# Kernel optimization log

Hardware: AMD Instinct MI355X
Metric: run time of the kernel (lower is better)

## Reference

```python
import jax, jax.numpy as jnp
import numpy as np

N = 100000   # nodes
E = 400000   # edges
L = 128      # latent_size
LN_EPS = 1e-5


def _mlp(x, W1, b1, W2, b2, g=None, beta=None):
    # build_mlp_d: Linear -> ReLU -> Linear, optional trailing LayerNorm
    h = jax.nn.relu(x @ W1 + b1)
    y = h @ W2 + b2
    if g is not None:
        mu = y.mean(-1, keepdims=True)
        var = y.var(-1, keepdims=True)
        y = (y - mu) / jnp.sqrt(var + LN_EPS) * g + beta
    return y


def setup_inputs():
    key = jax.random.key(0)
    ks = iter(jax.random.split(key, 100))

    def nrm(shape, scale=1.0):
        return jax.random.normal(next(ks), shape, jnp.float32) * scale

    inp = {}
    inp["edge_index"] = jax.random.randint(next(ks), (2, E), 0, N, dtype=jnp.int32)
    for nm in ["senders_pos", "receivers_pos", "edge_dx", "edge_dt",
               "vector_a", "vector_b", "vector_c",
               "senders_v_t", "senders_v_tm1", "senders_w_t",
               "receivers_v_t", "receivers_v_tm1", "receivers_w_t"]:
        inp[nm] = nrm((E, 3))
    inp["edge_attr"] = nrm((E, 1))
    inp["node_latent"] = nrm((N, L))

    def mlp_p(pref, din, dh, dout, ln):
        inp[pref + "_W1"] = nrm((din, dh), 1.0 / np.sqrt(din))
        inp[pref + "_b1"] = jnp.zeros((dh,), jnp.float32)
        inp[pref + "_W2"] = nrm((dh, dout), 1.0 / np.sqrt(dh))
        inp[pref + "_b2"] = jnp.zeros((dout,), jnp.float32)
        if ln:
            inp[pref + "_g"] = jnp.ones((dout,), jnp.float32)
            inp[pref + "_b"] = jnp.zeros((dout,), jnp.float32)

    mlp_p("ef", 9, L, L, True)       # edge_feat_encoder
    mlp_p("ee", 3, L, L, True)       # edge_encoder
    mlp_p("ie", 3 * L, L, L, True)   # interaction_encoder
    mlp_p("i1", L, L, 3, False)      # i1_decoder
    mlp_p("i2", L, L, 3, False)      # i2_decoder
    mlp_p("fs", L, L, 1, False)      # f_scaler
    mlp_p("nw", L, L, 1, False)      # node_weight_decoder
    mlp_p("mi", L, L, 1, False)      # m_inv_decoder
    mlp_p("ii", L, L, 1, False)      # i_inv_decoder
    mlp_p("de", L, L, 1, False)      # dv_ext_decoder
    # bias node weights to ~1 so the r0ij denominator stays away from 0
    inp["nw_b2"] = jnp.ones((1,), jnp.float32)
    return inp


def reference(edge_index, senders_pos, receivers_pos, edge_dx, edge_dt, edge_attr,
              vector_a, vector_b, vector_c,
              senders_v_t, senders_v_tm1, senders_w_t,
              receivers_v_t, receivers_v_tm1, receivers_w_t, node_latent,
              ef_W1, ef_b1, ef_W2, ef_b2, ef_g, ef_b,
              ee_W1, ee_b1, ee_W2, ee_b2, ee_g, ee_b,
              ie_W1, ie_b1, ie_W2, ie_b2, ie_g, ie_b,
              i1_W1, i1_b1, i1_W2, i1_b2,
              i2_W1, i2_b1, i2_W2, i2_b2,
              fs_W1, fs_b1, fs_W2, fs_b2,
              nw_W1, nw_b1, nw_W2, nw_b2,
              mi_W1, mi_b1, mi_W2, mi_b2,
              ii_W1, ii_b1, ii_W2, ii_b2,
              de_W1, de_b1, de_W2, de_b2):
    senders, receivers = edge_index[0], edge_index[1]

    def dots(v):  # [E,3] dotted against the three edge-frame basis vectors -> [E,3]
        return jnp.stack([jnp.einsum('ej,ej->e', v, vector_a),
                          jnp.einsum('ej,ej->e', v, vector_b),
                          jnp.einsum('ej,ej->e', v, vector_c)], axis=1)

    # --- InteractionEncoder ---
    senders_features = jnp.concatenate(
        [dots(senders_v_t), dots(senders_v_tm1), dots(senders_w_t)], axis=1)   # [E,9]
    receivers_features = -jnp.concatenate(
        [dots(receivers_v_t), dots(receivers_v_tm1), dots(receivers_w_t)], axis=1)  # [E,9]

    edge_in = jnp.concatenate(
        [jnp.linalg.norm(edge_dx, axis=1, keepdims=True),
         jnp.linalg.norm(edge_dt, axis=1, keepdims=True),
         edge_attr], axis=1)                                                    # [E,3]
    edge_latent = _mlp(edge_in, ee_W1, ee_b1, ee_W2, ee_b2, ee_g, ee_b)
    senders_latent = _mlp(senders_features, ef_W1, ef_b1, ef_W2, ef_b2, ef_g, ef_b)
    receivers_latent = _mlp(receivers_features, ef_W1, ef_b1, ef_W2, ef_b2, ef_g, ef_b)

    interaction_in = jnp.concatenate(
        [senders_latent + receivers_latent,
         node_latent[senders] + node_latent[receivers],
         edge_latent], axis=1)                                                  # [E,3L]
    interaction_latent = _mlp(interaction_in, ie_W1, ie_b1, ie_W2, ie_b2, ie_g, ie_b)

    # --- InteractionDecoder ---
    coeff_f = _mlp(interaction_latent, i1_W1, i1_b1, i1_W2, i1_b2)  # [E,3]
    coeff_a = _mlp(interaction_latent, i2_W1, i2_b1, i2_W2, i2_b2)  # [E,3]
    node_weights = _mlp(node_latent, nw_W1, nw_b1, nw_W2, nw_b2)    # [N,1]
    lambda_ij = _mlp(interaction_latent, fs_W1, fs_b1, fs_W2, fs_b2)  # [E,1]

    fij = coeff_f[:, 0:1] * vector_a + coeff_f[:, 1:2] * vector_b + coeff_f[:, 2:3] * vector_c
    aij = coeff_a[:, 0:1] * vector_a + coeff_a[:, 1:2] * vector_b + coeff_a[:, 2:3] * vector_c
    ws = node_weights[senders]
    wr = node_weights[receivers]
    r0ij = (ws * senders_pos + wr * receivers_pos) / (ws + wr)
    tauij = aij - jnp.cross(receivers_pos - r0ij, fij) * lambda_ij

    # --- Node_Internal_Dv_Decoder ---
    m_inv = _mlp(node_latent, mi_W1, mi_b1, mi_W2, mi_b2)  # [N,1]
    i_inv = _mlp(node_latent, ii_W1, ii_b1, ii_W2, ii_b2)  # [N,1]
    out_fij = jax.ops.segment_sum(fij, receivers, num_segments=N)   # scatter_add
    node_dv_int = m_inv * out_fij + _mlp(node_latent, de_W1, de_b1, de_W2, de_b2)
    out_tij = jax.ops.segment_sum(tauij, receivers, num_segments=N)
    node_dw_int = i_inv * out_tij

    return (node_dv_int, node_dw_int, interaction_latent)
```

## Files before the change

kernel.cpp:

```cpp
#include <hip/hip_runtime.h>
#include <hip/hip_fp16.h>
#include <stdint.h>

#define E_EDGES 400000
#define N_NODES 100000

#define OW1P  ((size_t)0)
#define OW2P  ((size_t)98304)
#define OW1D  ((size_t)131072)
#define OW2D  ((size_t)229376)
#define OW1E  ((size_t)241664)
#define OW2E  ((size_t)249856)
#define OW1C  ((size_t)282624)
#define OW2C  ((size_t)290816)
#define OSLR  ((size_t)524288)
#define ONW   (OSLR + (size_t)E_EDGES * 64 * 4)
#define OMI   (ONW + (size_t)N_NODES * 4)
#define OII   (OMI + (size_t)N_NODES * 4)
#define ODE   (OII + (size_t)N_NODES * 4)
#define OFS   (ODE + (size_t)N_NODES * 4)
#define OTS   (OFS + (size_t)N_NODES * 12)
#define WSEND (OTS + (size_t)N_NODES * 12)

typedef __attribute__((ext_vector_type(8))) _Float16 f16x8;
typedef __attribute__((ext_vector_type(4))) float f32x4;

__device__ __forceinline__ uint32_t f2h(float f) {
  return (uint32_t)__half_as_ushort(__float2half(f));
}
__device__ __forceinline__ float wave_sum64(float v) {
#pragma unroll
  for (int off = 32; off > 0; off >>= 1) v += __shfl_xor(v, off, 64);
  return v;
}

__device__ __forceinline__ void gemv8(const float* __restrict__ W,
                                      const float* __restrict__ xb, int xstride,
                                      int Ka, int lane, float* a0, float* a1) {
#pragma unroll 2
  for (int i = 0; i < Ka; i += 4) {
    float w0[4], w1[4];
#pragma unroll
    for (int u = 0; u < 4; ++u) {
      w0[u] = W[(size_t)(i + u) * 128 + lane];
      w1[u] = W[(size_t)(i + u) * 128 + 64 + lane];
    }
#pragma unroll
    for (int r = 0; r < 8; ++r) {
#pragma unroll
      for (int u = 0; u < 4; ++u) {
        float xv = xb[r * xstride + i + u];
        a0[r] = fmaf(xv, w0[u], a0[r]);
        a1[r] = fmaf(xv, w1[u], a1[r]);
      }
    }
  }
}

__device__ __forceinline__ void copy8x128(const float* __restrict__ src,
                                          float* __restrict__ dst, int lane) {
#pragma unroll
  for (int t = 0; t < 4; ++t) {
    float4 v = ((const float4*)src)[lane + 64 * t];
    ((float4*)dst)[lane + 64 * t] = v;
  }
}

__global__ __launch_bounds__(256) void k_node(
    const float* __restrict__ NL,
    const float* __restrict__ nw_W1, const float* __restrict__ nw_b1,
    const float* __restrict__ nw_W2, const float* __restrict__ nw_b2,
    const float* __restrict__ mi_W1, const float* __restrict__ mi_b1,
    const float* __restrict__ mi_W2, const float* __restrict__ mi_b2,
    const float* __restrict__ ii_W1, const float* __restrict__ ii_b1,
    const float* __restrict__ ii_W2, const float* __restrict__ ii_b2,
    const float* __restrict__ de_W1, const float* __restrict__ de_b1,
    const float* __restrict__ de_W2, const float* __restrict__ de_b2,
    float* __restrict__ o_nw, float* __restrict__ o_mi, float* __restrict__ o_ii,
    float* __restrict__ o_de) {
  __shared__ float xb[4][8 * 128];
  int w = threadIdx.x >> 6, l = threadIdx.x & 63;
  int nb = blockIdx.x * 32 + w * 8;
  copy8x128(NL + (size_t)nb * 128, xb[w], l);
  __syncthreads();
  const float* W1s[4] = {nw_W1, mi_W1, ii_W1, de_W1};
  const float* B1[4] = {nw_b1, mi_b1, ii_b1, de_b1};
  const float* W2[4] = {nw_W2, mi_W2, ii_W2, de_W2};
  const float* B2[4] = {nw_b2, mi_b2, ii_b2, de_b2};
  float* OUT[4] = {o_nw, o_mi, o_ii, o_de};
#pragma unroll
  for (int m = 0; m < 4; ++m) {
    float b10 = B1[m][l], b11 = B1[m][l + 64];
    float a0[8], a1[8];
#pragma unroll
    for (int r = 0; r < 8; ++r) { a0[r] = b10; a1[r] = b11; }
    gemv8(W1s[m], xb[w], 128, 128, l, a0, a1);
    float w2a = W2[m][l], w2b = W2[m][l + 64];
    float b2 = B2[m][0];
    float y[8];
#pragma unroll
    for (int r = 0; r < 8; ++r) {
      float p = fmaxf(a0[r], 0.f) * w2a + fmaxf(a1[r], 0.f) * w2b;
      y[r] = wave_sum64(p) + b2;
    }
    if (l == 0) {
#pragma unroll
      for (int r = 0; r < 8; ++r) OUT[m][nb + r] = y[r];
    }
  }
}

__global__ __launch_bounds__(256) void k_prep(
    const float* __restrict__ W1, const float* __restrict__ W2,
    const float* __restrict__ i1W1, const float* __restrict__ i2W1,
    const float* __restrict__ fsW1,
    const float* __restrict__ i1W2, const float* __restrict__ i2W2,
    const float* __restrict__ fsW2,
    const float* __restrict__ efW1, const float* __restrict__ efW2,
    const float* __restrict__ eeW1, const float* __restrict__ eeW2,
    unsigned short* __restrict__ W1P, unsigned short* __restrict__ W2P,
    unsigned short* __restrict__ W1D, unsigned short* __restrict__ W2D,
    unsigned short* __restrict__ W1E, unsigned short* __restrict__ W2E,
    unsigned short* __restrict__ W1C, unsigned short* __restrict__ W2C) {
  int i = blockIdx.x * 256 + threadIdx.x;
  if (i < 12 * 128 * 32) {
    int kin = i & 31, c = (i >> 5) & 127, ks = i >> 12;
    int kx = ks * 32 + kin;
    int ko = (kx < 128) ? ((kx & 1) * 64 + (kx >> 1)) : kx;
    W1P[i] = (unsigned short)f2h(W1[(size_t)ko * 128 + c]);
  }
  if (i < 4 * 128 * 32) {
    int kin = i & 31, c = (i >> 5) & 127, ks = i >> 12;
    W2P[i] = (unsigned short)f2h(W2[(size_t)(ks * 32 + kin) * 128 + c]);
  }
  if (i < 4 * 384 * 32) {
    int kin = i & 31;
    int rest = i >> 5;
    int c = rest % 384;
    int ks = rest / 384;
    int k = ks * 32 + kin;
    int head = c >> 7, ch = c & 127;
    const float* Wh = head == 0 ? i1W1 : head == 1 ? i2W1 : fsW1;
    W1D[i] = (unsigned short)f2h(Wh[(size_t)k * 128 + ch]);
  }
  if (i < 12 * 16 * 32) {
    int kin = i & 31;
    int rest = i >> 5;
    int col = rest & 15;
    int ks = rest >> 4;
    int k = ks * 32 + kin;
    float v = 0.f;
    if (k < 128) { if (col < 3) v = i1W2[(size_t)k * 3 + col]; }
    else if (k < 256) { if (col >= 3 && col < 6) v = i2W2[(size_t)(k - 128) * 3 + (col - 3)]; }
    else { if (col == 6) v = fsW2[k - 256]; }
    W2D[i] = (unsigned short)f2h(v);
  }
  if (i < 128 * 32) {
    int kin = i & 31, c = i >> 5;
    W1E[i] = (unsigned short)(kin < 9 ? f2h(efW1[(size_t)kin * 128 + c]) : 0);
  }
  if (i < 4 * 128 * 32) {
    int kin = i & 31, c = (i >> 5) & 127, ks = i >> 12;
    W2E[i] = (unsigned short)f2h(efW2[(size_t)(ks * 32 + kin) * 128 + c]);
  }
  if (i < 128 * 32) {
    int kin = i & 31, c = i >> 5;
    W1C[i] = (unsigned short)(kin < 3 ? f2h(eeW1[(size_t)kin * 128 + c]) : 0);
  }
  if (i < 4 * 128 * 32) {
    int kin = i & 31, c = (i >> 5) & 127, ks = i >> 12;
    W2C[i] = (unsigned short)f2h(eeW2[(size_t)(ks * 32 + kin) * 128 + c]);
  }
}

#define EFY 0
#define EFX 16896
#define EFH 19456
__global__ __launch_bounds__(256) void k_ef_mfma(
    const float* __restrict__ va, const float* __restrict__ vb, const float* __restrict__ vc,
    const float* __restrict__ svt, const float* __restrict__ svtm1, const float* __restrict__ swt,
    const float* __restrict__ rvt, const float* __restrict__ rvtm1, const float* __restrict__ rwt,
    const unsigned short* __restrict__ W1E, const unsigned short* __restrict__ W2E,
    const float* __restrict__ b1, const float* __restrict__ b2,
    const float* __restrict__ g, const float* __restrict__ be, uint32_t* __restrict__ slrp) {
  __shared__ uint8_t lds[27648];
  int tid = threadIdx.x;
  int w = tid >> 6, l = tid & 63;
  int lrow = l & 15, lk = l >> 4;
  int base = blockIdx.x * 16;

  if (tid < 32) {
    int row = tid;
    int e = base + (row & 15);
    bool isR = row >= 16;
    const float* p0 = isR ? rvt : svt;
    const float* p1 = isR ? rvtm1 : svtm1;
    const float* p2 = isR ? rwt : swt;
    float sgn = isR ? -1.f : 1.f;
    float ax = va[e * 3], ay = va[e * 3 + 1], az = va[e * 3 + 2];
    float bx = vb[e * 3], by = vb[e * 3 + 1], bz = vb[e * 3 + 2];
    float cx = vc[e * 3], cy = vc[e * 3 + 1], cz = vc[e * 3 + 2];
    float f[10];
    const float* ps[3] = {p0, p1, p2};
#pragma unroll
    for (int q = 0; q < 3; ++q) {
      float vx = ps[q][e * 3], vy = ps[q][e * 3 + 1], vz = ps[q][e * 3 + 2];
      f[q * 3 + 0] = sgn * (vx * ax + vy * ay + vz * az);
      f[q * 3 + 1] = sgn * (vx * bx + vy * by + vz * bz);
      f[q * 3 + 2] = sgn * (vx * cx + vy * cy + vz * cz);
    }
    f[9] = 0.f;
    uint32_t* xr = (uint32_t*)(lds + EFX + (uint32_t)row * 80);
#pragma unroll
    for (int j = 0; j < 5; ++j) xr[j] = f2h(f[2 * j]) | (f2h(f[2 * j + 1]) << 16);
#pragma unroll
    for (int j = 5; j < 16; ++j) xr[j] = 0;
  }

  int wc = w * 32;
  f16x8 w2f[4][2];
#pragma unroll
  for (int ks = 0; ks < 4; ++ks)
#pragma unroll
    for (int ct = 0; ct < 2; ++ct)
      w2f[ks][ct] = *(const f16x8*)(W2E + ((size_t)(ks * 128 + wc + ct * 16 + lrow) * 32 + lk * 8));
  float b1c0 = b1[wc + lrow], b1c1 = b1[wc + 16 + lrow];
  float b2c0 = b2[wc + lrow], b2c1 = b2[wc + 16 + lrow];
  f16x8 bf0 = *(const f16x8*)(W1E + ((size_t)(wc + lrow) * 32 + lk * 8));
  f16x8 bf1 = *(const f16x8*)(W1E + ((size_t)(wc + 16 + lrow) * 32 + lk * 8));
  __syncthreads();

  f32x4 a1[2][2];
#pragma unroll
  for (int rt = 0; rt < 2; ++rt) {
    int row = rt * 16 + lrow;
    f16x8 af = *(const f16x8*)(lds + EFX + (uint32_t)row * 80 + lk * 16);
    a1[rt][0] = __builtin_amdgcn_mfma_f32_16x16x32_f16(af, bf0, (f32x4){0.f,0.f,0.f,0.f}, 0, 0, 0);
    a1[rt][1] = __builtin_amdgcn_mfma_f32_16x16x32_f16(af, bf1, (f32x4){0.f,0.f,0.f,0.f}, 0, 0, 0);
  }
#pragma unroll
  for (int rt = 0; rt < 2; ++rt)
#pragma unroll
    for (int ct = 0; ct < 2; ++ct) {
      float bc = ct ? b1c1 : b1c0;
      int col = wc + ct * 16 + lrow;
#pragma unroll
      for (int q = 0; q < 4; ++q) {
        int row = rt * 16 + lk * 4 + q;
        float h = fmaxf(a1[rt][ct][q] + bc, 0.f);
        uint32_t bo = ((uint32_t)row * 256 + (uint32_t)col * 2) ^ ((uint32_t)(row & 7) << 4);
        *(unsigned short*)(lds + EFH + bo) = (unsigned short)f2h(h);
      }
    }
  __syncthreads();

  f32x4 a2[2][2];
#pragma unroll
  for (int rt = 0; rt < 2; ++rt)
#pragma unroll
    for (int ct = 0; ct < 2; ++ct) a2[rt][ct] = (f32x4){0.f, 0.f, 0.f, 0.f};
#pragma unroll
  for (int ks = 0; ks < 4; ++ks) {
#pragma unroll
    for (int rt = 0; rt < 2; ++rt) {
      int row = rt * 16 + lrow;
      uint32_t bo = ((uint32_t)row * 256 + (uint32_t)(ks * 64 + lk * 16)) ^ ((uint32_t)(row & 7) << 4);
      f16x8 af = *(const f16x8*)(lds + EFH + bo);
      a2[rt][0] = __builtin_amdgcn_mfma_f32_16x16x32_f16(af, w2f[ks][0], a2[rt][0], 0, 0, 0);
      a2[rt][1] = __builtin_amdgcn_mfma_f32_16x16x32_f16(af, w2f[ks][1], a2[rt][1], 0, 0, 0);
    }
  }
  float* Ys = (float*)(lds + EFY);
#pragma unroll
  for (int rt = 0; rt < 2; ++rt)
#pragma unroll
    for (int ct = 0; ct < 2; ++ct) {
      float bc = ct ? b2c1 : b2c0;
      int col = wc + ct * 16 + lrow;
#pragma unroll
      for (int q = 0; q < 4; ++q) {
        int row = rt * 16 + lk * 4 + q;
        Ys[row * 132 + col] = a2[rt][ct][q] + bc;
      }
    }
  __syncthreads();

  float gl0 = g[l], gl1 = g[l + 64], bl0 = be[l], bl1 = be[l + 64];
#pragma unroll
  for (int r8 = 0; r8 < 8; ++r8) {
    int row = w * 8 + r8;
    float y0 = Ys[row * 132 + l], y1 = Ys[row * 132 + 64 + l];
    float s = wave_sum64(y0 + y1);
    float s2 = wave_sum64(y0 * y0 + y1 * y1);
    float mu = s * 0.0078125f;
    float var = s2 * 0.0078125f - mu * mu;
    float rstd = rsqrtf(var + 1e-5f);
    Ys[row * 132 + l] = (y0 - mu) * rstd * gl0 + bl0;
    Ys[row * 132 + 64 + l] = (y1 - mu) * rstd * gl1 + bl1;
  }
  __syncthreads();
  if (w < 2) {
#pragma unroll
    for (int r8 = 0; r8 < 8; ++r8) {
      int row = w * 8 + r8;
      float s0 = Ys[row * 132 + l] + Ys[(row + 16) * 132 + l];
      float s1 = Ys[row * 132 + 64 + l] + Ys[(row + 16) * 132 + 64 + l];
      slrp[(size_t)(base + row) * 64 + l] = f2h(s0) | (f2h(s1) << 16);
    }
  }
}

#define XI 0
#define HH 24576
#define XE 32768
#define EIX 35328
__global__ __launch_bounds__(256) void k_ie_fused(
    const int* __restrict__ ei, const float* __restrict__ NL,
    const uint32_t* __restrict__ slrp,
    const float* __restrict__ dxp, const float* __restrict__ dtp, const float* __restrict__ attr,
    const unsigned short* __restrict__ W1C, const unsigned short* __restrict__ W2C,
    const float* __restrict__ eb1, const float* __restrict__ eb2,
    const float* __restrict__ eg, const float* __restrict__ ebe,
    const unsigned short* __restrict__ W1P, const unsigned short* __restrict__ W2P,
    const float* __restrict__ b1, const float* __restrict__ b2,
    const float* __restrict__ g, const float* __restrict__ be,
    float* __restrict__ il) {
  __shared__ uint8_t lds[35584];
  int tid = threadIdx.x;
  int w = tid >> 6, l = tid & 63;
  int lrow = l & 15, lk = l >> 4;
  int base = blockIdx.x * 32;
  int wc = w * 32;

  int* eis = (int*)(lds + EIX);
  int* eit = eis + 32;
  if (tid < 32) {
    eis[tid] = ei[base + tid];
    eit[tid] = ei[E_EDGES + base + tid];
    int e = base + tid;
    float a0 = dxp[e * 3], a1v = dxp[e * 3 + 1], a2 = dxp[e * 3 + 2];
    float t0 = dtp[e * 3], t1 = dtp[e * 3 + 1], t2 = dtp[e * 3 + 2];
    float f0 = sqrtf(a0 * a0 + a1v * a1v + a2 * a2);
    float f1 = sqrtf(t0 * t0 + t1 * t1 + t2 * t2);
    float f2v = attr[e];
    uint32_t* xr = (uint32_t*)(lds + XE + (uint32_t)tid * 80);
    xr[0] = f2h(f0) | (f2h(f1) << 16);
    xr[1] = f2h(f2v);
#pragma unroll
    for (int j = 2; j < 16; ++j) xr[j] = 0;
  }

  f16x8 w2fe[4][2];
#pragma unroll
  for (int ks = 0; ks < 4; ++ks)
#pragma unroll
    for (int ct = 0; ct < 2; ++ct)
      w2fe[ks][ct] = *(const f16x8*)(W2C + ((size_t)(ks * 128 + wc + ct * 16 + lrow) * 32 + lk * 8));
  float eb1c0 = eb1[wc + lrow], eb1c1 = eb1[wc + 16 + lrow];
  float eb2c0 = eb2[wc + lrow], eb2c1 = eb2[wc + 16 + lrow];
  f16x8 bfe0 = *(const f16x8*)(W1C + ((size_t)(wc + lrow) * 32 + lk * 8));
  f16x8 bfe1 = *(const f16x8*)(W1C + ((size_t)(wc + 16 + lrow) * 32 + lk * 8));
  __syncthreads();

  f32x4 aE[2][2];
#pragma unroll
  for (int rt = 0; rt < 2; ++rt) {
    int row = rt * 16 + lrow;
    f16x8 af = *(const f16x8*)(lds + XE + (uint32_t)row * 80 + lk * 16);
    aE[rt][0] = __builtin_amdgcn_mfma_f32_16x16x32_f16(af, bfe0, (f32x4){0.f,0.f,0.f,0.f}, 0, 0, 0);
    aE[rt][1] = __builtin_amdgcn_mfma_f32_16x16x32_f16(af, bfe1, (f32x4){0.f,0.f,0.f,0.f}, 0, 0, 0);
  }
#pragma unroll
  for (int rt = 0; rt < 2; ++rt)
#pragma unroll
    for (int ct = 0; ct < 2; ++ct) {
      float bc = ct ? eb1c1 : eb1c0;
      int col = wc + ct * 16 + lrow;
#pragma unroll
      for (int q = 0; q < 4; ++q) {
        int row = rt * 16 + lk * 4 + q;
        float h = fmaxf(aE[rt][ct][q] + bc, 0.f);
        uint32_t bo = ((uint32_t)row * 256 + (uint32_t)col * 2) ^ ((uint32_t)(row & 7) << 4);
        *(unsigned short*)(lds + HH + bo) = (unsigned short)f2h(h);
      }
    }
  __syncthreads();

  f32x4 aE2[2][2];
#pragma unroll
  for (int rt = 0; rt < 2; ++rt)
#pragma unroll
    for (int ct = 0; ct < 2; ++ct) aE2[rt][ct] = (f32x4){0.f, 0.f, 0.f, 0.f};
#pragma unroll
  for (int ks = 0; ks < 4; ++ks) {
#pragma unroll
    for (int rt = 0; rt < 2; ++rt) {
      int row = rt * 16 + lrow;
      uint32_t bo = ((uint32_t)row * 256 + (uint32_t)(ks * 64 + lk * 16)) ^ ((uint32_t)(row & 7) << 4);
      f16x8 af = *(const f16x8*)(lds + HH + bo);
      aE2[rt][0] = __builtin_amdgcn_mfma_f32_16x16x32_f16(af, w2fe[ks][0], aE2[rt][0], 0, 0, 0);
      aE2[rt][1] = __builtin_amdgcn_mfma_f32_16x16x32_f16(af, w2fe[ks][1], aE2[rt][1], 0, 0, 0);
    }
  }
  float* Ys = (float*)(lds + XI);
#pragma unroll
  for (int rt = 0; rt < 2; ++rt)
#pragma unroll
    for (int ct = 0; ct < 2; ++ct) {
      float bc = ct ? eb2c1 : eb2c0;
      int col = wc + ct * 16 + lrow;
#pragma unroll
      for (int q = 0; q < 4; ++q) {
        int row = rt * 16 + lk * 4 + q;
        Ys[row * 132 + col] = aE2[rt][ct][q] + bc;
      }
    }
  __syncthreads();

  float el0[8], el1[8];
  {
    float gl0 = eg[l], gl1 = eg[l + 64], bl0 = ebe[l], bl1 = ebe[l + 64];
#pragma unroll
    for (int r8 = 0; r8 < 8; ++r8) {
      int row = w * 8 + r8;
      float y0 = Ys[row * 132 + l], y1 = Ys[row * 132 + 64 + l];
      float s = wave_sum64(y0 + y1);
      float s2 = wave_sum64(y0 * y0 + y1 * y1);
      float mu = s * 0.0078125f;
      float var = s2 * 0.0078125f - mu * mu;
      float rstd = rsqrtf(var + 1e-5f);
      el0[r8] = (y0 - mu) * rstd * gl0 + bl0;
      el1[r8] = (y1 - mu) * rstd * gl1 + bl1;
    }
  }
  __syncthreads();

#pragma unroll
  for (int i = tid; i < 32 * 64; i += 256) {
    int r = i >> 6, c = i & 63;
    uint32_t bo = ((uint32_t)r * 768 + (uint32_t)c * 4) ^ ((uint32_t)(r & 7) << 4);
    *(uint32_t*)(lds + XI + bo) = slrp[(size_t)(base + r) * 64 + c];
  }
  const float2* NL2 = (const float2*)NL;
#pragma unroll
  for (int i = tid; i < 32 * 64; i += 256) {
    int r = i >> 6, c = i & 63;
    float2 a = NL2[(size_t)eis[r] * 64 + c];
    float2 bq = NL2[(size_t)eit[r] * 64 + c];
    uint32_t p = f2h(a.x + bq.x) | (f2h(a.y + bq.y) << 16);
    uint32_t bo = ((uint32_t)r * 768 + 256u + (uint32_t)c * 4) ^ ((uint32_t)(r & 7) << 4);
    *(uint32_t*)(lds + XI + bo) = p;
  }
#pragma unroll
  for (int r8 = 0; r8 < 8; ++r8) {
    int row = w * 8 + r8;
    uint32_t bo0 = ((uint32_t)row * 768 + 512u + (uint32_t)l * 2) ^ ((uint32_t)(row & 7) << 4);
    uint32_t bo1 = ((uint32_t)row * 768 + 512u + (uint32_t)(l + 64) * 2) ^ ((uint32_t)(row & 7) << 4);
    *(unsigned short*)(lds + XI + bo0) = (unsigned short)f2h(el0[r8]);
    *(unsigned short*)(lds + XI + bo1) = (unsigned short)f2h(el1[r8]);
  }

  f16x8 w2f[4][2];
#pragma unroll
  for (int ks = 0; ks < 4; ++ks)
#pragma unroll
    for (int ct = 0; ct < 2; ++ct)
      w2f[ks][ct] = *(const f16x8*)(W2P + ((size_t)(ks * 128 + wc + ct * 16 + lrow) * 32 + lk * 8));
  float b1c0 = b1[wc + lrow], b1c1 = b1[wc + 16 + lrow];
  float b2c0 = b2[wc + lrow], b2c1 = b2[wc + 16 + lrow];
  __syncthreads();

  f32x4 acc[2][2];
#pragma unroll
  for (int rt = 0; rt < 2; ++rt)
#pragma unroll
    for (int ct = 0; ct < 2; ++ct) acc[rt][ct] = (f32x4){0.f, 0.f, 0.f, 0.f};
#pragma unroll 2
  for (int ks = 0; ks < 12; ++ks) {
    f16x8 bf0 = *(const f16x8*)(W1P + ((size_t)(ks * 128 + wc + lrow) * 32 + lk * 8));
    f16x8 bf1 = *(const f16x8*)(W1P + ((size_t)(ks * 128 + wc + 16 + lrow) * 32 + lk * 8));
#pragma unroll
    for (int rt = 0; rt < 2; ++rt) {
      int row = rt * 16 + lrow;
      uint32_t bo = ((uint32_t)row * 768 + (uint32_t)(ks * 64 + lk * 16)) ^ ((uint32_t)(row & 7) << 4);
      f16x8 af = *(const f16x8*)(lds + XI + bo);
      acc[rt][0] = __builtin_amdgcn_mfma_f32_16x16x32_f16(af, bf0, acc[rt][0], 0, 0, 0);
      acc[rt][1] = __builtin_amdgcn_mfma_f32_16x16x32_f16(af, bf1, acc[rt][1], 0, 0, 0);
    }
  }
#pragma unroll
  for (int rt = 0; rt < 2; ++rt)
#pragma unroll
    for (int ct = 0; ct < 2; ++ct) {
      float bc = ct ? b1c1 : b1c0;
      int col = wc + ct * 16 + lrow;
#pragma unroll
      for (int q = 0; q < 4; ++q) {
        int row = rt * 16 + lk * 4 + q;
        float h = fmaxf(acc[rt][ct][q] + bc, 0.f);
        uint32_t bo = ((uint32_t)row * 256 + (uint32_t)col * 2) ^ ((uint32_t)(row & 7) << 4);
        *(unsigned short*)(lds + HH + bo) = (unsigned short)f2h(h);
      }
    }
  __syncthreads();

  f32x4 acc2[2][2];
#pragma unroll
  for (int rt = 0; rt < 2; ++rt)
#pragma unroll
    for (int ct = 0; ct < 2; ++ct) acc2[rt][ct] = (f32x4){0.f, 0.f, 0.f, 0.f};
#pragma unroll
  for (int ks = 0; ks < 4; ++ks) {
#pragma unroll
    for (int rt = 0; rt < 2; ++rt) {
      int row = rt * 16 + lrow;
      uint32_t bo = ((uint32_t)row * 256 + (uint32_t)(ks * 64 + lk * 16)) ^ ((uint32_t)(row & 7) << 4);
      f16x8 af = *(const f16x8*)(lds + HH + bo);
      acc2[rt][0] = __builtin_amdgcn_mfma_f32_16x16x32_f16(af, w2f[ks][0], acc2[rt][0], 0, 0, 0);
      acc2[rt][1] = __builtin_amdgcn_mfma_f32_16x16x32_f16(af, w2f[ks][1], acc2[rt][1], 0, 0, 0);
    }
  }
#pragma unroll
  for (int rt = 0; rt < 2; ++rt)
#pragma unroll
    for (int ct = 0; ct < 2; ++ct) {
      float bc = ct ? b2c1 : b2c0;
      int col = wc + ct * 16 + lrow;
#pragma unroll
      for (int q = 0; q < 4; ++q) {
        int row = rt * 16 + lk * 4 + q;
        Ys[row * 132 + col] = acc2[rt][ct][q] + bc;
      }
    }
  __syncthreads();

  float gl0 = g[l], gl1 = g[l + 64], bl0 = be[l], bl1 = be[l + 64];
#pragma unroll
  for (int r8 = 0; r8 < 8; ++r8) {
    int row = w * 8 + r8;
    float y0 = Ys[row * 132 + l], y1 = Ys[row * 132 + 64 + l];
    float s = wave_sum64(y0 + y1);
    float s2 = wave_sum64(y0 * y0 + y1 * y1);
    float mu = s * 0.0078125f;
    float var = s2 * 0.0078125f - mu * mu;
    float rstd = rsqrtf(var + 1e-5f);
    size_t o = (size_t)(base + row) * 128;
    il[o + l] = (y0 - mu) * rstd * gl0 + bl0;
    il[o + 64 + l] = (y1 - mu) * rstd * gl1 + bl1;
  }
}

__global__ __launch_bounds__(256) void k_dec_mfma(
    const int* __restrict__ ei, const float* __restrict__ il,
    const unsigned short* __restrict__ W1D, const unsigned short* __restrict__ W2D,
    const float* __restrict__ i1b1, const float* __restrict__ i2b1,
    const float* __restrict__ fsb1,
    const float* __restrict__ i1b2, const float* __restrict__ i2b2,
    const float* __restrict__ fsb2,
    const float* __restrict__ nw, const float* __restrict__ spos, const float* __restrict__ rpos,
    const float* __restrict__ va, const float* __restrict__ vb, const float* __restrict__ vc,
    float* __restrict__ fsum, float* __restrict__ tsum) {
  __shared__ uint8_t lds[32768];
  int tid = threadIdx.x;
  int w = tid >> 6, l = tid & 63;
  int lrow = l & 15, lk = l >> 4;
  int base = blockIdx.x * 32;

  const float2* IL2 = (const float2*)il;
#pragma unroll
  for (int i = tid; i < 32 * 64; i += 256) {
    int r = i >> 6, c = i & 63;
    float2 a = IL2[(size_t)(base + r) * 64 + c];
    uint32_t p = f2h(a.x) | (f2h(a.y) << 16);
    uint32_t bo = ((uint32_t)r * 256 + (uint32_t)c * 4) ^ ((uint32_t)(r & 7) << 4);
    *(uint32_t*)(lds + 24576 + bo) = p;
  }

  float b1c[6];
#pragma unroll
  for (int ct = 0; ct < 6; ++ct) {
    int c = w * 96 + ct * 16 + lrow;
    const float* bsel = (c < 128) ? i1b1 : (c < 256) ? i2b1 : fsb1;
    b1c[ct] = bsel[c & 127];
  }
  f16x8 w2f[12];
#pragma unroll
  for (int ks = 0; ks < 12; ++ks)
    w2f[ks] = *(const f16x8*)(W2D + ((size_t)(ks * 16 + lrow) * 32 + lk * 8));
  float b2c = lrow < 3 ? i1b2[lrow] : lrow < 6 ? i2b2[lrow - 3] : lrow == 6 ? fsb2[0] : 0.f;
  __syncthreads();

  f32x4 acc[2][6];
#pragma unroll
  for (int rt = 0; rt < 2; ++rt)
#pragma unroll
    for (int ct = 0; ct < 6; ++ct) acc[rt][ct] = (f32x4){0.f, 0.f, 0.f, 0.f};
#pragma unroll
  for (int ks = 0; ks < 4; ++ks) {
    f16x8 bf[6];
#pragma unroll
    for (int ct = 0; ct < 6; ++ct)
      bf[ct] = *(const f16x8*)(W1D + ((size_t)(ks * 384 + w * 96 + ct * 16 + lrow) * 32 + lk * 8));
#pragma unroll
    for (int rt = 0; rt < 2; ++rt) {
      int row = rt * 16 + lrow;
      uint32_t bo = ((uint32_t)row * 256 + (uint32_t)(ks * 64 + lk * 16)) ^ ((uint32_t)(row & 7) << 4);
      f16x8 af = *(const f16x8*)(lds + 24576 + bo);
#pragma unroll
      for (int ct = 0; ct < 6; ++ct)
        acc[rt][ct] = __builtin_amdgcn_mfma_f32_16x16x32_f16(af, bf[ct], acc[rt][ct], 0, 0, 0);
    }
  }
#pragma unroll
  for (int rt = 0; rt < 2; ++rt)
#pragma unroll
    for (int ct = 0; ct < 6; ++ct) {
      int col = w * 96 + ct * 16 + lrow;
#pragma unroll
      for (int q = 0; q < 4; ++q) {
        int row = rt * 16 + lk * 4 + q;
        float h = fmaxf(acc[rt][ct][q] + b1c[ct], 0.f);
        uint32_t bo = ((uint32_t)row * 768 + (uint32_t)col * 2) ^ ((uint32_t)(row & 7) << 4);
        *(unsigned short*)(lds + bo) = (unsigned short)f2h(h);
      }
    }
  __syncthreads();

  float* Ys = (float*)(lds + 24576);
  if (w < 2) {
    f32x4 acc2 = (f32x4){0.f, 0.f, 0.f, 0.f};
#pragma unroll
    for (int ks = 0; ks < 12; ++ks) {
      int row = w * 16 + lrow;
      uint32_t bo = ((uint32_t)row * 768 + (uint32_t)(ks * 64 + lk * 16)) ^ ((uint32_t)(row & 7) << 4);
      f16x8 af = *(const f16x8*)(lds + bo);
      acc2 = __builtin_amdgcn_mfma_f32_16x16x32_f16(af, w2f[ks], acc2, 0, 0, 0);
    }
#pragma unroll
    for (int q = 0; q < 4; ++q) {
      int row = w * 16 + lk * 4 + q;
      Ys[row * 17 + lrow] = acc2[q] + b2c;
    }
  }
  __syncthreads();

  if (tid < 32) {
    int e = base + tid;
    int s = ei[e], t = ei[E_EDGES + e];
    float cf0 = Ys[tid * 17 + 0], cf1 = Ys[tid * 17 + 1], cf2 = Ys[tid * 17 + 2];
    float ca0 = Ys[tid * 17 + 3], ca1 = Ys[tid * 17 + 4], ca2 = Ys[tid * 17 + 5];
    float lam = Ys[tid * 17 + 6];
    float ax = va[e * 3], ay = va[e * 3 + 1], az = va[e * 3 + 2];
    float bx = vb[e * 3], by = vb[e * 3 + 1], bz = vb[e * 3 + 2];
    float cx = vc[e * 3], cy = vc[e * 3 + 1], cz = vc[e * 3 + 2];
    float fx = cf0 * ax + cf1 * bx + cf2 * cx;
    float fy = cf0 * ay + cf1 * by + cf2 * cy;
    float fz = cf0 * az + cf1 * bz + cf2 * cz;
    float gx = ca0 * ax + ca1 * bx + ca2 * cx;
    float gy = ca0 * ay + ca1 * by + ca2 * cy;
    float gz = ca0 * az + ca1 * bz + ca2 * cz;
    float wsn = nw[s], wrn = nw[t];
    float sx = spos[e * 3], sy = spos[e * 3 + 1], sz = spos[e * 3 + 2];
    float rx = rpos[e * 3], ry = rpos[e * 3 + 1], rz = rpos[e * 3 + 2];
    float inv = 1.f / (wsn + wrn);
    float r0x = (wsn * sx + wrn * rx) * inv;
    float r0y = (wsn * sy + wrn * ry) * inv;
    float r0z = (wsn * sz + wrn * rz) * inv;
    float ddx = rx - r0x, ddy = ry - r0y, ddz = rz - r0z;
    float cxx = ddy * fz - ddz * fy;
    float cyy = ddz * fx - ddx * fz;
    float czz = ddx * fy - ddy * fx;
    float tx = gx - cxx * lam, ty = gy - cyy * lam, tz = gz - czz * lam;
    atomicAdd(&fsum[(size_t)t * 3 + 0], fx);
    atomicAdd(&fsum[(size_t)t * 3 + 1], fy);
    atomicAdd(&fsum[(size_t)t * 3 + 2], fz);
    atomicAdd(&tsum[(size_t)t * 3 + 0], tx);
    atomicAdd(&tsum[(size_t)t * 3 + 1], ty);
    atomicAdd(&tsum[(size_t)t * 3 + 2], tz);
  }
}

__global__ __launch_bounds__(256) void k_final(const float* __restrict__ mi,
                                               const float* __restrict__ ii,
                                               const float* __restrict__ de,
                                               const float* __restrict__ fsum,
                                               const float* __restrict__ tsum,
                                               float* __restrict__ out) {
  int n = blockIdx.x * 256 + threadIdx.x;
  if (n >= N_NODES) return;
  float m = mi[n], iv = ii[n], d = de[n];
#pragma unroll
  for (int c = 0; c < 3; ++c) {
    out[(size_t)n * 3 + c] = m * fsum[(size_t)n * 3 + c] + d;
    out[(size_t)3 * N_NODES + (size_t)n * 3 + c] = iv * tsum[(size_t)n * 3 + c];
  }
}

extern "C" void kernel_launch(void* const* d_in, const int* in_sizes, int n_in, void* d_out,
                              int out_size, void* d_ws, size_t ws_size, hipStream_t stream) {
  if (ws_size < WSEND) return;

  const int* ei = (const int*)d_in[0];
  const float* spos = (const float*)d_in[1];
  const float* rpos = (const float*)d_in[2];
  const float* dx = (const float*)d_in[3];
  const float* dt = (const float*)d_in[4];
  const float* va = (const float*)d_in[5];
  const float* vb = (const float*)d_in[6];
  const float* vc = (const float*)d_in[7];
  const float* svt = (const float*)d_in[8];
  const float* svtm1 = (const float*)d_in[9];
  const float* swt = (const float*)d_in[10];
  const float* rvt = (const float*)d_in[11];
  const float* rvtm1 = (const float*)d_in[12];
  const float* rwt = (const float*)d_in[13];
  const float* attr = (const float*)d_in[14];
  const float* NL = (const float*)d_in[15];
  const float* ef_W1 = (const float*)d_in[16];
  const float* ef_b1 = (const float*)d_in[17];
  const float* ef_W2 = (const float*)d_in[18];
  const float* ef_b2 = (const float*)d_in[19];
  const float* ef_g = (const float*)d_in[20];
  const float* ef_b = (const float*)d_in[21];
  const float* ee_W1 = (const float*)d_in[22];
  const float* ee_b1 = (const float*)d_in[23];
  const float* ee_W2 = (const float*)d_in[24];
  const float* ee_b2 = (const float*)d_in[25];
  const float* ee_g = (const float*)d_in[26];
  const float* ee_b = (const float*)d_in[27];
  const float* ie_W1 = (const float*)d_in[28];
  const float* ie_b1 = (const float*)d_in[29];
  const float* ie_W2 = (const float*)d_in[30];
  const float* ie_b2 = (const float*)d_in[31];
  const float* ie_g = (const float*)d_in[32];
  const float* ie_b = (const float*)d_in[33];
  const float* i1_W1 = (const float*)d_in[34];
  const float* i1_b1 = (const float*)d_in[35];
  const float* i1_W2 = (const float*)d_in[36];
  const float* i1_b2 = (const float*)d_in[37];
  const float* i2_W1 = (const float*)d_in[38];
  const float* i2_b1 = (const float*)d_in[39];
  const float* i2_W2 = (const float*)d_in[40];
  const float* i2_b2 = (const float*)d_in[41];
  const float* fs_W1 = (const float*)d_in[42];
  const float* fs_b1 = (const float*)d_in[43];
  const float* fs_W2 = (const float*)d_in[44];
  const float* fs_b2 = (const float*)d_in[45];
  const float* nw_W1 = (const float*)d_in[46];
  const float* nw_b1 = (const float*)d_in[47];
  const float* nw_W2 = (const float*)d_in[48];
  const float* nw_b2 = (const float*)d_in[49];
  const float* mi_W1 = (const float*)d_in[50];
  const float* mi_b1 = (const float*)d_in[51];
  const float* mi_W2 = (const float*)d_in[52];
  const float* mi_b2 = (const float*)d_in[53];
  const float* ii_W1 = (const float*)d_in[54];
  const float* ii_b1 = (const float*)d_in[55];
  const float* ii_W2 = (const float*)d_in[56];
  const float* ii_b2 = (const float*)d_in[57];
  const float* de_W1 = (const float*)d_in[58];
  const float* de_b1 = (const float*)d_in[59];
  const float* de_W2 = (const float*)d_in[60];
  const float* de_b2 = (const float*)d_in[61];

  float* out = (float*)d_out;
  char* ws = (char*)d_ws;
  unsigned short* W1P = (unsigned short*)(ws + OW1P);
  unsigned short* W2P = (unsigned short*)(ws + OW2P);
  unsigned short* W1D = (unsigned short*)(ws + OW1D);
  unsigned short* W2D = (unsigned short*)(ws + OW2D);
  unsigned short* W1E = (unsigned short*)(ws + OW1E);
  unsigned short* W2E = (unsigned short*)(ws + OW2E);
  unsigned short* W1C = (unsigned short*)(ws + OW1C);
  unsigned short* W2C = (unsigned short*)(ws + OW2C);
  uint32_t* slrp = (uint32_t*)(ws + OSLR);
  float* o_nw = (float*)(ws + ONW);
  float* o_mi = (float*)(ws + OMI);
  float* o_ii = (float*)(ws + OII);
  float* o_de = (float*)(ws + ODE);
  float* fsum = (float*)(ws + OFS);
  float* tsum = (float*)(ws + OTS);
  float* il = out + 6 * N_NODES;

  hipMemsetAsync(ws + OFS, 0, (size_t)N_NODES * 24, stream);

  hipLaunchKernelGGL(k_prep, dim3(192), dim3(256), 0, stream, ie_W1, ie_W2,
                     i1_W1, i2_W1, fs_W1, i1_W2, i2_W2, fs_W2,
                     ef_W1, ef_W2, ee_W1, ee_W2,
                     W1P, W2P, W1D, W2D, W1E, W2E, W1C, W2C);

  hipLaunchKernelGGL(k_node, dim3(N_NODES / 32), dim3(256), 0, stream, NL,
                     nw_W1, nw_b1, nw_W2, nw_b2, mi_W1, mi_b1, mi_W2, mi_b2,
                     ii_W1, ii_b1, ii_W2, ii_b2, de_W1, de_b1, de_W2, de_b2,
                     o_nw, o_mi, o_ii, o_de);

  hipLaunchKernelGGL(k_ef_mfma, dim3(E_EDGES / 16), dim3(256), 0, stream, va, vb, vc,
                     svt, svtm1, swt, rvt, rvtm1, rwt,
                     W1E, W2E, ef_b1, ef_b2, ef_g, ef_b, slrp);

  hipLaunchKernelGGL(k_ie_fused, dim3(E_EDGES / 32), dim3(256), 0, stream, ei, NL, slrp,
                     dx, dt, attr, W1C, W2C, ee_b1, ee_b2, ee_g, ee_b,
                     W1P, W2P, ie_b1, ie_b2, ie_g, ie_b, il);

  hipLaunchKernelGGL(k_dec_mfma, dim3(E_EDGES / 32), dim3(256), 0, stream, ei, il,
                     W1D, W2D, i1_b1, i2_b1, fs_b1, i1_b2, i2_b2, fs_b2,
                     o_nw, spos, rpos, va, vb, vc, fsum, tsum);

  hipLaunchKernelGGL(k_final, dim3((N_NODES + 255) / 256), dim3(256), 0, stream, o_mi, o_ii, o_de,
                     fsum, tsum, out);
}
```

Before: 1.216 ms.

## Fuse decoder MLPs into interaction encoder kernel and split node MLPs per wave

The decoder stage (i1/i2/fs MLPs, force/torque computation and scatter) now runs inside the interaction-encoder kernel. It reads the layer-normed latent straight from LDS as fp16 instead of reloading it from global memory in a separate launch, and edge indices come from LDS as well. This removes one kernel launch and the global re-read of the E×128 latent, at the cost of more registers and LDS pressure in a larger kernel. Separately, in the node kernel each wave now computes one of the four MLPs over all 32 nodes rather than all four MLPs over 8 nodes, so each wave keeps one weight set.

```diff
diff --git a/kernel.cpp b/kernel.cpp
--- a/kernel.cpp
+++ b/kernel.cpp
@@ -80,23 +80,25 @@
     float* __restrict__ o_de) {
   __shared__ float xb[4][8 * 128];
   int w = threadIdx.x >> 6, l = threadIdx.x & 63;
-  int nb = blockIdx.x * 32 + w * 8;
-  copy8x128(NL + (size_t)nb * 128, xb[w], l);
+  int nb0 = blockIdx.x * 32;
+  copy8x128(NL + (size_t)(nb0 + w * 8) * 128, xb[w], l);
   __syncthreads();
   const float* W1s[4] = {nw_W1, mi_W1, ii_W1, de_W1};
   const float* B1[4] = {nw_b1, mi_b1, ii_b1, de_b1};
   const float* W2[4] = {nw_W2, mi_W2, ii_W2, de_W2};
   const float* B2[4] = {nw_b2, mi_b2, ii_b2, de_b2};
   float* OUT[4] = {o_nw, o_mi, o_ii, o_de};
-#pragma unroll
-  for (int m = 0; m < 4; ++m) {
-    float b10 = B1[m][l], b11 = B1[m][l + 64];
+  const float* W1w = W1s[w];
+  float b10 = B1[w][l], b11 = B1[w][l + 64];
+  float w2a = W2[w][l], w2b = W2[w][l + 64];
+  float b2 = B2[w][0];
+  float* OUTw = OUT[w];
+#pragma unroll
+  for (int gidx = 0; gidx < 4; ++gidx) {
     float a0[8], a1[8];
 #pragma unroll
     for (int r = 0; r < 8; ++r) { a0[r] = b10; a1[r] = b11; }
-    gemv8(W1s[m], xb[w], 128, 128, l, a0, a1);
-    float w2a = W2[m][l], w2b = W2[m][l + 64];
-    float b2 = B2[m][0];
+    gemv8(W1w, xb[gidx], 128, 128, l, a0, a1);
     float y[8];
 #pragma unroll
     for (int r = 0; r < 8; ++r) {
@@ -105,7 +107,7 @@
     }
     if (l == 0) {
 #pragma unroll
-      for (int r = 0; r < 8; ++r) OUT[m][nb + r] = y[r];
+      for (int r = 0; r < 8; ++r) OUTw[nb0 + gidx * 8 + r] = y[r];
     }
   }
 }
@@ -324,7 +326,14 @@
     const unsigned short* __restrict__ W1P, const unsigned short* __restrict__ W2P,
     const float* __restrict__ b1, const float* __restrict__ b2,
     const float* __restrict__ g, const float* __restrict__ be,
-    float* __restrict__ il) {
+    const unsigned short* __restrict__ W1D, const unsigned short* __restrict__ W2D,
+    const float* __restrict__ i1b1, const float* __restrict__ i2b1,
+    const float* __restrict__ fsb1,
+    const float* __restrict__ i1b2, const float* __restrict__ i2b2,
+    const float* __restrict__ fsb2,
+    const float* __restrict__ nw, const float* __restrict__ spos, const float* __restrict__ rpos,
+    const float* __restrict__ va, const float* __restrict__ vb, const float* __restrict__ vc,
+    float* __restrict__ il, float* __restrict__ fsum, float* __restrict__ tsum) {
   __shared__ uint8_t lds[35584];
   int tid = threadIdx.x;
   int w = tid >> 6, l = tid & 63;
@@ -534,67 +543,43 @@
     }
   __syncthreads();
 
-  float gl0 = g[l], gl1 = g[l + 64], bl0 = be[l], bl1 = be[l + 64];
-#pragma unroll
-  for (int r8 = 0; r8 < 8; ++r8) {
-    int row = w * 8 + r8;
-    float y0 = Ys[row * 132 + l], y1 = Ys[row * 132 + 64 + l];
-    float s = wave_sum64(y0 + y1);
-    float s2 = wave_sum64(y0 * y0 + y1 * y1);
-    float mu = s * 0.0078125f;
-    float var = s2 * 0.0078125f - mu * mu;
-    float rstd = rsqrtf(var + 1e-5f);
-    size_t o = (size_t)(base + row) * 128;
-    il[o + l] = (y0 - mu) * rstd * gl0 + bl0;
-    il[o + 64 + l] = (y1 - mu) * rstd * gl1 + bl1;
-  }
-}
-
-__global__ __launch_bounds__(256) void k_dec_mfma(
-    const int* __restrict__ ei, const float* __restrict__ il,
-    const unsigned short* __restrict__ W1D, const unsigned short* __restrict__ W2D,
-    const float* __restrict__ i1b1, const float* __restrict__ i2b1,
-    const float* __restrict__ fsb1,
-    const float* __restrict__ i1b2, const float* __restrict__ i2b2,
-    const float* __restrict__ fsb2,
-    const float* __restrict__ nw, const float* __restrict__ spos, const float* __restrict__ rpos,
-    const float* __restrict__ va, const float* __restrict__ vb, const float* __restrict__ vc,
-    float* __restrict__ fsum, float* __restrict__ tsum) {
-  __shared__ uint8_t lds[32768];
-  int tid = threadIdx.x;
-  int w = tid >> 6, l = tid & 63;
-  int lrow = l & 15, lk = l >> 4;
-  int base = blockIdx.x * 32;
-
-  const float2* IL2 = (const float2*)il;
-#pragma unroll
-  for (int i = tid; i < 32 * 64; i += 256) {
-    int r = i >> 6, c = i & 63;
-    float2 a = IL2[(size_t)(base + r) * 64 + c];
-    uint32_t p = f2h(a.x) | (f2h(a.y) << 16);
-    uint32_t bo = ((uint32_t)r * 256 + (uint32_t)c * 4) ^ ((uint32_t)(r & 7) << 4);
-    *(uint32_t*)(lds + 24576 + bo) = p;
-  }
-
-  float b1c[6];
+  {
+    float gl0 = g[l], gl1 = g[l + 64], bl0 = be[l], bl1 = be[l + 64];
+#pragma unroll
+    for (int r8 = 0; r8 < 8; ++r8) {
+      int row = w * 8 + r8;
+      float y0 = Ys[row * 132 + l], y1 = Ys[row * 132 + 64 + l];
+      float s = wave_sum64(y0 + y1);
+      float s2 = wave_sum64(y0 * y0 + y1 * y1);
+      float mu = s * 0.0078125f;
+      float var = s2 * 0.0078125f - mu * mu;
+      float rstd = rsqrtf(var + 1e-5f);
+      float o0 = (y0 - mu) * rstd * gl0 + bl0;
+      float o1 = (y1 - mu) * rstd * gl1 + bl1;
+      size_t o = (size_t)(base + row) * 128;
+      il[o + l] = o0;
+      il[o + 64 + l] = o1;
+      uint32_t bx0 = ((uint32_t)row * 256 + (uint32_t)l * 2) ^ ((uint32_t)(row & 7) << 4);
+      uint32_t bx1 = ((uint32_t)row * 256 + (uint32_t)(l + 64) * 2) ^ ((uint32_t)(row & 7) << 4);
+      *(unsigned short*)(lds + HH + bx0) = (unsigned short)f2h(o0);
+      *(unsigned short*)(lds + HH + bx1) = (unsigned short)f2h(o1);
+    }
+  }
+
+  float db1c[6];
 #pragma unroll
   for (int ct = 0; ct < 6; ++ct) {
     int c = w * 96 + ct * 16 + lrow;
     const float* bsel = (c < 128) ? i1b1 : (c < 256) ? i2b1 : fsb1;
-    b1c[ct] = bsel[c & 127];
-  }
-  f16x8 w2f[12];
-#pragma unroll
-  for (int ks = 0; ks < 12; ++ks)
-    w2f[ks] = *(const f16x8*)(W2D + ((size_t)(ks * 16 + lrow) * 32 + lk * 8));
-  float b2c = lrow < 3 ? i1b2[lrow] : lrow < 6 ? i2b2[lrow - 3] : lrow == 6 ? fsb2[0] : 0.f;
-  __syncthreads();
-
-  f32x4 acc[2][6];
-#pragma unroll
-  for (int rt = 0; rt < 2; ++rt)
-#pragma unroll
-    for (int ct = 0; ct < 6; ++ct) acc[rt][ct] = (f32x4){0.f, 0.f, 0.f, 0.f};
+    db1c[ct] = bsel[c & 127];
+  }
+  __syncthreads();
+
+  f32x4 dacc[2][6];
+#pragma unroll
+  for (int rt = 0; rt < 2; ++rt)
+#pragma unroll
+    for (int ct = 0; ct < 6; ++ct) dacc[rt][ct] = (f32x4){0.f, 0.f, 0.f, 0.f};
 #pragma unroll
   for (int ks = 0; ks < 4; ++ks) {
     f16x8 bf[6];
@@ -605,10 +590,10 @@
     for (int rt = 0; rt < 2; ++rt) {
       int row = rt * 16 + lrow;
       uint32_t bo = ((uint32_t)row * 256 + (uint32_t)(ks * 64 + lk * 16)) ^ ((uint32_t)(row & 7) << 4);
-      f16x8 af = *(const f16x8*)(lds + 24576 + bo);
+      f16x8 af = *(const f16x8*)(lds + HH + bo);
 #pragma unroll
       for (int ct = 0; ct < 6; ++ct)
-        acc[rt][ct] = __builtin_amdgcn_mfma_f32_16x16x32_f16(af, bf[ct], acc[rt][ct], 0, 0, 0);
+        dacc[rt][ct] = __builtin_amdgcn_mfma_f32_16x16x32_f16(af, bf[ct], dacc[rt][ct], 0, 0, 0);
     }
   }
 #pragma unroll
@@ -619,37 +604,42 @@
 #pragma unroll
       for (int q = 0; q < 4; ++q) {
         int row = rt * 16 + lk * 4 + q;
-        float h = fmaxf(acc[rt][ct][q] + b1c[ct], 0.f);
+        float h = fmaxf(dacc[rt][ct][q] + db1c[ct], 0.f);
         uint32_t bo = ((uint32_t)row * 768 + (uint32_t)col * 2) ^ ((uint32_t)(row & 7) << 4);
-        *(unsigned short*)(lds + bo) = (unsigned short)f2h(h);
+        *(unsigned short*)(lds + XI + bo) = (unsigned short)f2h(h);
       }
     }
   __syncthreads();
 
-  float* Ys = (float*)(lds + 24576);
+  float* Ys2 = (float*)(lds + HH);
   if (w < 2) {
-    f32x4 acc2 = (f32x4){0.f, 0.f, 0.f, 0.f};
+    f16x8 dw2f[12];
+#pragma unroll
+    for (int ks = 0; ks < 12; ++ks)
+      dw2f[ks] = *(const f16x8*)(W2D + ((size_t)(ks * 16 + lrow) * 32 + lk * 8));
+    float db2c = lrow < 3 ? i1b2[lrow] : lrow < 6 ? i2b2[lrow - 3] : lrow == 6 ? fsb2[0] : 0.f;
+    f32x4 dacc2 = (f32x4){0.f, 0.f, 0.f, 0.f};
 #pragma unroll
     for (int ks = 0; ks < 12; ++ks) {
       int row = w * 16 + lrow;
       uint32_t bo = ((uint32_t)row * 768 + (uint32_t)(ks * 64 + lk * 16)) ^ ((uint32_t)(row & 7) << 4);
-      f16x8 af = *(const f16x8*)(lds + bo);
-      acc2 = __builtin_amdgcn_mfma_f32_16x16x32_f16(af, w2f[ks], acc2, 0, 0, 0);
+      f16x8 af = *(const f16x8*)(lds + XI + bo);
+      dacc2 = __builtin_amdgcn_mfma_f32_16x16x32_f16(af, dw2f[ks], dacc2, 0, 0, 0);
     }
 #pragma unroll
     for (int q = 0; q < 4; ++q) {
       int row = w * 16 + lk * 4 + q;
-      Ys[row * 17 + lrow] = acc2[q] + b2c;
+      Ys2[row * 17 + lrow] = dacc2[q] + db2c;
     }
   }
   __syncthreads();
 
   if (tid < 32) {
     int e = base + tid;
-    int s = ei[e], t = ei[E_EDGES + e];
-    float cf0 = Ys[tid * 17 + 0], cf1 = Ys[tid * 17 + 1], cf2 = Ys[tid * 17 + 2];
-    float ca0 = Ys[tid * 17 + 3], ca1 = Ys[tid * 17 + 4], ca2 = Ys[tid * 17 + 5];
-    float lam = Ys[tid * 17 + 6];
+    int s = eis[tid], t = eit[tid];
+    float cf0 = Ys2[tid * 17 + 0], cf1 = Ys2[tid * 17 + 1], cf2 = Ys2[tid * 17 + 2];
+    float ca0 = Ys2[tid * 17 + 3], ca1 = Ys2[tid * 17 + 4], ca2 = Ys2[tid * 17 + 5];
+    float lam = Ys2[tid * 17 + 6];
     float ax = va[e * 3], ay = va[e * 3 + 1], az = va[e * 3 + 2];
     float bx = vb[e * 3], by = vb[e * 3 + 1], bz = vb[e * 3 + 2];
     float cx = vc[e * 3], cy = vc[e * 3 + 1], cz = vc[e * 3 + 2];
@@ -800,11 +790,9 @@
 
   hipLaunchKernelGGL(k_ie_fused, dim3(E_EDGES / 32), dim3(256), 0, stream, ei, NL, slrp,
                      dx, dt, attr, W1C, W2C, ee_b1, ee_b2, ee_g, ee_b,
-                     W1P, W2P, ie_b1, ie_b2, ie_g, ie_b, il);
-
-  hipLaunchKernelGGL(k_dec_mfma, dim3(E_EDGES / 32), dim3(256), 0, stream, ei, il,
+                     W1P, W2P, ie_b1, ie_b2, ie_g, ie_b,
                      W1D, W2D, i1_b1, i2_b1, fs_b1, i1_b2, i2_b2, fs_b2,
-                     o_nw, spos, rpos, va, vb, vc, fsum, tsum);
+                     o_nw, spos, rpos, va, vb, vc, il, fsum, tsum);
 
   hipLaunchKernelGGL(k_final, dim3((N_NODES + 255) / 256), dim3(256), 0, stream, o_mi, o_ii, o_de,
                      fsum, tsum, out);
```

Result: slower. 1.249 ms (+2.7%).

## Merge node MLP kernel into edge-feature kernel and shrink ie LDS footprint

Applied to the files above, without the earlier changes.

Folds the node decoder MLPs into the edge-feature encoder launch as extra trailing blocks, removing one kernel launch and letting node work fill the tail of the edge grid. Node blocks now assign one MLP per wave across all 32 nodes instead of each wave running all four MLPs on its own 8 nodes, which keeps that MLP's weights in one wave. In k_ie_fused the edge index staging in LDS is dropped in favour of direct global reads, and the XE region is moved so LDS use falls from 35584 to 32768 bytes, aiming at higher occupancy. The trade-off is redundant index loads per thread and a larger, branchier kernel whose register use is set by the heavier MFMA path.

```diff
diff --git a/kernel.cpp b/kernel.cpp
--- a/kernel.cpp
+++ b/kernel.cpp
@@ -4,6 +4,8 @@
 
 #define E_EDGES 400000
 #define N_NODES 100000
+#define EF_BLOCKS (E_EDGES / 16)
+#define NODE_BLOCKS (N_NODES / 32)
 
 #define OW1P  ((size_t)0)
 #define OW2P  ((size_t)98304)
@@ -63,50 +65,6 @@
   for (int t = 0; t < 4; ++t) {
     float4 v = ((const float4*)src)[lane + 64 * t];
     ((float4*)dst)[lane + 64 * t] = v;
-  }
-}
-
-__global__ __launch_bounds__(256) void k_node(
-    const float* __restrict__ NL,
-    const float* __restrict__ nw_W1, const float* __restrict__ nw_b1,
-    const float* __restrict__ nw_W2, const float* __restrict__ nw_b2,
-    const float* __restrict__ mi_W1, const float* __restrict__ mi_b1,
-    const float* __restrict__ mi_W2, const float* __restrict__ mi_b2,
-    const float* __restrict__ ii_W1, const float* __restrict__ ii_b1,
-    const float* __restrict__ ii_W2, const float* __restrict__ ii_b2,
-    const float* __restrict__ de_W1, const float* __restrict__ de_b1,
-    const float* __restrict__ de_W2, const float* __restrict__ de_b2,
-    float* __restrict__ o_nw, float* __restrict__ o_mi, float* __restrict__ o_ii,
-    float* __restrict__ o_de) {
-  __shared__ float xb[4][8 * 128];
-  int w = threadIdx.x >> 6, l = threadIdx.x & 63;
-  int nb = blockIdx.x * 32 + w * 8;
-  copy8x128(NL + (size_t)nb * 128, xb[w], l);
-  __syncthreads();
-  const float* W1s[4] = {nw_W1, mi_W1, ii_W1, de_W1};
-  const float* B1[4] = {nw_b1, mi_b1, ii_b1, de_b1};
-  const float* W2[4] = {nw_W2, mi_W2, ii_W2, de_W2};
-  const float* B2[4] = {nw_b2, mi_b2, ii_b2, de_b2};
-  float* OUT[4] = {o_nw, o_mi, o_ii, o_de};
-#pragma unroll
-  for (int m = 0; m < 4; ++m) {
-    float b10 = B1[m][l], b11 = B1[m][l + 64];
-    float a0[8], a1[8];
-#pragma unroll
-    for (int r = 0; r < 8; ++r) { a0[r] = b10; a1[r] = b11; }
-    gemv8(W1s[m], xb[w], 128, 128, l, a0, a1);
-    float w2a = W2[m][l], w2b = W2[m][l + 64];
-    float b2 = B2[m][0];
-    float y[8];
-#pragma unroll
-    for (int r = 0; r < 8; ++r) {
-      float p = fmaxf(a0[r], 0.f) * w2a + fmaxf(a1[r], 0.f) * w2b;
-      y[r] = wave_sum64(p) + b2;
-    }
-    if (l == 0) {
-#pragma unroll
-      for (int r = 0; r < 8; ++r) OUT[m][nb + r] = y[r];
-    }
   }
 }
 
@@ -176,16 +134,64 @@
 #define EFY 0
 #define EFX 16896
 #define EFH 19456
-__global__ __launch_bounds__(256) void k_ef_mfma(
+__global__ __launch_bounds__(256) void k_pre(
     const float* __restrict__ va, const float* __restrict__ vb, const float* __restrict__ vc,
     const float* __restrict__ svt, const float* __restrict__ svtm1, const float* __restrict__ swt,
     const float* __restrict__ rvt, const float* __restrict__ rvtm1, const float* __restrict__ rwt,
     const unsigned short* __restrict__ W1E, const unsigned short* __restrict__ W2E,
     const float* __restrict__ b1, const float* __restrict__ b2,
-    const float* __restrict__ g, const float* __restrict__ be, uint32_t* __restrict__ slrp) {
+    const float* __restrict__ g, const float* __restrict__ be,
+    uint32_t* __restrict__ slrp,
+    const float* __restrict__ NL,
+    const float* __restrict__ nw_W1, const float* __restrict__ nw_b1,
+    const float* __restrict__ nw_W2, const float* __restrict__ nw_b2,
+    const float* __restrict__ mi_W1, const float* __restrict__ mi_b1,
+    const float* __restrict__ mi_W2, const float* __restrict__ mi_b2,
+    const float* __restrict__ ii_W1, const float* __restrict__ ii_b1,
+    const float* __restrict__ ii_W2, const float* __restrict__ ii_b2,
+    const float* __restrict__ de_W1, const float* __restrict__ de_b1,
+    const float* __restrict__ de_W2, const float* __restrict__ de_b2,
+    float* __restrict__ o_nw, float* __restrict__ o_mi, float* __restrict__ o_ii,
+    float* __restrict__ o_de) {
   __shared__ uint8_t lds[27648];
   int tid = threadIdx.x;
   int w = tid >> 6, l = tid & 63;
+
+  if (blockIdx.x >= EF_BLOCKS) {
+    float (*xb)[1024] = (float(*)[1024])lds;
+    int nb0 = (blockIdx.x - EF_BLOCKS) * 32;
+    copy8x128(NL + (size_t)(nb0 + w * 8) * 128, xb[w], l);
+    __syncthreads();
+    const float* W1s[4] = {nw_W1, mi_W1, ii_W1, de_W1};
+    const float* B1[4] = {nw_b1, mi_b1, ii_b1, de_b1};
+    const float* W2[4] = {nw_W2, mi_W2, ii_W2, de_W2};
+    const float* B2[4] = {nw_b2, mi_b2, ii_b2, de_b2};
+    float* OUT[4] = {o_nw, o_mi, o_ii, o_de};
+    const float* W1w = W1s[w];
+    float b10 = B1[w][l], b11 = B1[w][l + 64];
+    float w2a = W2[w][l], w2b = W2[w][l + 64];
+    float b2s = B2[w][0];
+    float* OUTw = OUT[w];
+#pragma unroll
+    for (int gidx = 0; gidx < 4; ++gidx) {
+      float a0[8], a1[8];
+#pragma unroll
+      for (int r = 0; r < 8; ++r) { a0[r] = b10; a1[r] = b11; }
+      gemv8(W1w, xb[gidx], 128, 128, l, a0, a1);
+      float y[8];
+#pragma unroll
+      for (int r = 0; r < 8; ++r) {
+        float p = fmaxf(a0[r], 0.f) * w2a + fmaxf(a1[r], 0.f) * w2b;
+        y[r] = wave_sum64(p) + b2s;
+      }
+      if (l == 0) {
+#pragma unroll
+        for (int r = 0; r < 8; ++r) OUTw[nb0 + gidx * 8 + r] = y[r];
+      }
+    }
+    return;
+  }
+
   int lrow = l & 15, lk = l >> 4;
   int base = blockIdx.x * 16;
 
@@ -311,9 +317,8 @@
 }
 
 #define XI 0
+#define XE 16896
 #define HH 24576
-#define XE 32768
-#define EIX 35328
 __global__ __launch_bounds__(256) void k_ie_fused(
     const int* __restrict__ ei, const float* __restrict__ NL,
     const uint32_t* __restrict__ slrp,
@@ -325,18 +330,14 @@
     const float* __restrict__ b1, const float* __restrict__ b2,
     const float* __restrict__ g, const float* __restrict__ be,
     float* __restrict__ il) {
-  __shared__ uint8_t lds[35584];
+  __shared__ uint8_t lds[32768];
   int tid = threadIdx.x;
   int w = tid >> 6, l = tid & 63;
   int lrow = l & 15, lk = l >> 4;
   int base = blockIdx.x * 32;
   int wc = w * 32;
 
-  int* eis = (int*)(lds + EIX);
-  int* eit = eis + 32;
   if (tid < 32) {
-    eis[tid] = ei[base + tid];
-    eit[tid] = ei[E_EDGES + base + tid];
     int e = base + tid;
     float a0 = dxp[e * 3], a1v = dxp[e * 3 + 1], a2 = dxp[e * 3 + 2];
     float t0 = dtp[e * 3], t1 = dtp[e * 3 + 1], t2 = dtp[e * 3 + 2];
@@ -445,8 +446,9 @@
 #pragma unroll
   for (int i = tid; i < 32 * 64; i += 256) {
     int r = i >> 6, c = i & 63;
-    float2 a = NL2[(size_t)eis[r] * 64 + c];
-    float2 bq = NL2[(size_t)eit[r] * 64 + c];
+    int s = ei[base + r], t = ei[E_EDGES + base + r];
+    float2 a = NL2[(size_t)s * 64 + c];
+    float2 bq = NL2[(size_t)t * 64 + c];
     uint32_t p = f2h(a.x + bq.x) | (f2h(a.y + bq.y) << 16);
     uint32_t bo = ((uint32_t)r * 768 + 256u + (uint32_t)c * 4) ^ ((uint32_t)(r & 7) << 4);
     *(uint32_t*)(lds + XI + bo) = p;
@@ -789,14 +791,12 @@
                      ef_W1, ef_W2, ee_W1, ee_W2,
                      W1P, W2P, W1D, W2D, W1E, W2E, W1C, W2C);
 
-  hipLaunchKernelGGL(k_node, dim3(N_NODES / 32), dim3(256), 0, stream, NL,
-                     nw_W1, nw_b1, nw_W2, nw_b2, mi_W1, mi_b1, mi_W2, mi_b2,
+  hipLaunchKernelGGL(k_pre, dim3(EF_BLOCKS + NODE_BLOCKS), dim3(256), 0, stream,
+                     va, vb, vc, svt, svtm1, swt, rvt, rvtm1, rwt,
+                     W1E, W2E, ef_b1, ef_b2, ef_g, ef_b, slrp,
+                     NL, nw_W1, nw_b1, nw_W2, nw_b2, mi_W1, mi_b1, mi_W2, mi_b2,
                      ii_W1, ii_b1, ii_W2, ii_b2, de_W1, de_b1, de_W2, de_b2,
                      o_nw, o_mi, o_ii, o_de);
-
-  hipLaunchKernelGGL(k_ef_mfma, dim3(E_EDGES / 16), dim3(256), 0, stream, va, vb, vc,
-                     svt, svtm1, swt, rvt, rvtm1, rwt,
-                     W1E, W2E, ef_b1, ef_b2, ef_g, ef_b, slrp);
 
   hipLaunchKernelGGL(k_ie_fused, dim3(E_EDGES / 32), dim3(256), 0, stream, ei, NL, slrp,
                      dx, dt, attr, W1C, W2C, ee_b1, ee_b2, ee_g, ee_b,
```

New measurement: 1.250 ms. 2.9% more time.
